# Optimization experiments

Measured on AMD Instinct MI355X. Metric: run time of the kernel, lower is better.

Reference implementation:

```python
import jax, jax.numpy as jnp
import numpy as np
from jax.scipy.special import logsumexp

B, T, D = 16, 512, 768
S, H, O = 4, 48, 48
EMISS_W = 0.5  # args.emiss_nn_weight


def setup_inputs() -> dict:
    key = jax.random.key(0)
    ks = jax.random.split(key, 6)
    emb = jax.random.normal(ks[0], (B, T, D), jnp.float32)
    # obs must be valid per-source distributions over n_obs (log is taken)
    obs = jax.nn.softmax(2.0 * jax.random.normal(ks[1], (B, T, S, O), jnp.float32), axis=-1)
    # default prior init: priors = 0.001, priors[0] = 1, param = log(priors)
    p = jnp.full((H,), 0.001, jnp.float32).at[0].set(1.0)
    state_priors = jnp.log(p)
    unnorm_trans = jax.random.normal(ks[2], (H, H), jnp.float32)
    unnorm_emiss = jnp.zeros((S, H, O), jnp.float32)
    # xavier_uniform with relu gain for the per-source emission Linears
    bound = np.sqrt(2.0) * np.sqrt(6.0 / (D + H * O))
    W_emiss = jax.random.uniform(ks[3], (S, H * O, D), jnp.float32, -bound, bound)
    b_emiss = jnp.zeros((S, H * O), jnp.float32)
    seq_lengths = jax.random.randint(ks[4], (B,), T // 2, T + 1).astype(jnp.int32)
    seq_lengths = seq_lengths.at[0].set(T)  # max length == T
    return dict(emb=emb, obs=obs, state_priors=state_priors, unnorm_trans=unnorm_trans,
                unnorm_emiss=unnorm_emiss, W_emiss=W_emiss, b_emiss=b_emiss,
                seq_lengths=seq_lengths)


def _lognorm(x):
    return x - logsumexp(x, axis=-1, keepdims=True)


def reference(emb, obs, state_priors, unnorm_trans, unnorm_emiss, W_emiss, b_emiss, seq_lengths):
    lp = jax.nn.log_softmax(state_priors)                 # [H]
    log_trans = jax.nn.log_softmax(unnorm_trans, axis=-1)  # [H,H] (constant over b,t)
    emiss = jax.nn.softmax(unnorm_emiss, axis=-1)          # [S,H,O]

    # neural emissions: per-source Linear(d_emb -> H*O), softmax over O
    logits = jnp.einsum('btd,sod->btso', emb, W_emiss) + b_emiss  # [B,T,S,H*O]
    nn_emiss = jax.nn.softmax(logits.reshape(B, T, S, H, O), axis=-1)
    # (nn_trans is computed by NeuralModule in the original but discarded)

    log_emiss = jnp.log((1.0 - EMISS_W) * emiss[None, None] + EMISS_W * nn_emiss)  # [B,T,S,H,O]
    # log_matmul over obs axis, then sum over sources -> [B,T,H]
    lep = logsumexp(log_emiss + jnp.log(obs)[:, :, :, None, :], axis=-1).sum(axis=2)

    # forward recursion (normalized each step)
    a0 = _lognorm(lp + lep[:, 0])                          # [B,H]

    def fstep(a_prev, lep_t):
        a = _lognorm(lep_t + logsumexp(a_prev[:, :, None] + log_trans[None], axis=1))
        return a, a

    _, alphas = jax.lax.scan(fstep, a0, jnp.swapaxes(lep[:, 1:], 0, 1))
    log_alpha = jnp.concatenate([a0[:, None], jnp.swapaxes(alphas, 0, 1)], axis=1)  # [B,T,H]

    # backward recursion: beta[t] = logsumexp_j(trans[i,j] + lep[t,j] + beta[t+1,j])
    bT = jnp.zeros((B, H), lep.dtype)

    def bstep(b_next, lep_t):
        b = logsumexp(log_trans[None] + (lep_t + b_next)[:, None, :], axis=2)
        return b, b

    _, betas = jax.lax.scan(bstep, bT, jnp.swapaxes(lep[:, :T - 1], 0, 1), reverse=True)
    log_beta = jnp.concatenate([jnp.swapaxes(betas, 0, 1), bT[:, None]], axis=1)  # [B,T,H]
    # per-example roll by (length - T) along time, as in the original
    log_beta = jax.vmap(lambda b, s: jnp.roll(b, s, axis=0))(log_beta, seq_lengths - T)

    log_gamma = _lognorm(log_alpha + log_beta)             # [B,T,H]

    # xi_t = trans + alpha[t-1] (outer-sum) (lep[t] + beta[t]),  t = 1..T-1
    xi = (log_trans[None, None]
          + log_alpha[:, :-1, :, None]
          + (lep[:, 1:] + log_beta[:, 1:])[:, :, None, :])  # [B,T-1,H,H]
    xi = xi - logsumexp(xi, axis=(-2, -1), keepdims=True)

    log_prior = jnp.mean(jnp.sum(jnp.exp(log_gamma[:, 0]) * lp, axis=-1))

    tran_terms = jnp.sum(jnp.exp(xi) * log_trans[None, None], axis=(-2, -1))  # [B,T-1]
    mask_tr = (jnp.arange(T - 1)[None] < (seq_lengths - 1)[:, None]).astype(lep.dtype)
    log_tran = jnp.mean(jnp.sum(tran_terms * mask_tr, axis=1))

    emis_terms = jnp.sum(jnp.exp(log_gamma) * lep, axis=-1)  # [B,T]
    mask_em = (jnp.arange(T)[None] < seq_lengths[:, None]).astype(lep.dtype)
    log_emis = jnp.mean(jnp.sum(emis_terms * mask_em, axis=1))

    return log_prior + log_tran + log_emis
```

## Files before the change

kernel.cpp:

```cpp
#include <hip/hip_runtime.h>
#include <math.h>

namespace {

constexpr int Bn = 16, Tn = 512, Dn = 768, Sn = 4, Hn = 48, On = 48;
constexpr int Mn = Bn * Tn;
constexpr int Gn = Sn * Hn;
constexpr int Nn = Gn * On;
constexpr float EMISS_W = 0.5f;

constexpr size_t OFF_LP   = 0;
constexpr size_t OFF_LT   = 64;
constexpr size_t OFF_PT   = OFF_LT + Hn*Hn;
constexpr size_t OFF_EM   = OFF_PT + Hn*Hn;
constexpr size_t OFF_LEPP = OFF_EM + (size_t)Sn*Hn*On;
constexpr size_t OFF_LEP  = OFF_LEPP + (size_t)Mn*Gn;
constexpr size_t OFF_LA   = OFF_LEP + (size_t)Mn*Hn;
constexpr size_t OFF_LB   = OFF_LA + (size_t)Mn*Hn;
constexpr size_t OFF_RED  = OFF_LB + (size_t)Mn*Hn;
constexpr size_t FLOATS_END = OFF_RED + (size_t)Mn;

typedef __attribute__((ext_vector_type(8))) short short8;
typedef __attribute__((ext_vector_type(4))) float f32x4;

__device__ inline float waveSum(float v){
#pragma unroll
  for (int o = 32; o; o >>= 1) v += __shfl_xor(v, o);
  return v;
}

__device__ inline unsigned short f2bf(float f){
  unsigned int u = __float_as_uint(f);
  u += 0x7FFFu + ((u >> 16) & 1u);
  return (unsigned short)(u >> 16);
}

__device__ inline void gload_lds16(const void* g, void* l){
  __builtin_amdgcn_global_load_lds(
      (const __attribute__((address_space(1))) void*)g,
      (__attribute__((address_space(3))) void*)l, 16, 0, 0);
}

__global__ void conv_kernel(const float* __restrict__ srcA, unsigned short* __restrict__ dstA,
                            int n4a,
                            const float* __restrict__ srcB, unsigned short* __restrict__ dstB,
                            int n4b){
  int i = blockIdx.x * blockDim.x + threadIdx.x;
  const float* s; unsigned short* d; int k;
  if (i < n4a){ s = srcA; d = dstA; k = i; }
  else { k = i - n4a; if (k >= n4b) return; s = srcB; d = dstB; }
  float4 v = ((const float4*)s)[k];
  ushort4 r;
  r.x = f2bf(v.x); r.y = f2bf(v.y); r.z = f2bf(v.z); r.w = f2bf(v.w);
  ((ushort4*)d)[k] = r;
}

__global__ void prep_kernel(const float* __restrict__ sp, const float* __restrict__ ut,
                            const float* __restrict__ ue, float* __restrict__ ws){
  int tid = threadIdx.x;
  float m = -INFINITY;
  for (int h = 0; h < Hn; ++h) m = fmaxf(m, sp[h]);
  float s = 0.f;
  for (int h = 0; h < Hn; ++h) s += __expf(sp[h] - m);
  float lse = m + __logf(s);
  if (tid < Hn) ws[OFF_LP + tid] = sp[tid] - lse;
  if (tid < Hn){
    const float* row = ut + tid * Hn;
    float mm = -INFINITY;
    for (int j = 0; j < Hn; ++j) mm = fmaxf(mm, row[j]);
    float ss = 0.f;
    for (int j = 0; j < Hn; ++j) ss += __expf(row[j] - mm);
    float l = mm + __logf(ss);
    for (int j = 0; j < Hn; ++j){
      float v = row[j] - l;
      ws[OFF_LT + tid*Hn + j] = v;
      ws[OFF_PT + tid*Hn + j] = __expf(v);
    }
  }
  for (int r = tid; r < Sn*Hn; r += blockDim.x){
    const float* row = ue + (size_t)r * On;
    float mm = -INFINITY;
    for (int o = 0; o < On; ++o) mm = fmaxf(mm, row[o]);
    float ss = 0.f;
    for (int o = 0; o < On; ++o) ss += __expf(row[o] - mm);
    float inv = 1.f/ss;
    for (int o = 0; o < On; ++o) ws[OFF_EM + (size_t)r*On + o] = __expf(row[o]-mm)*inv;
  }
}

constexpr int MT = 128, NT2 = 96, KT = 64;

__global__ __launch_bounds__(256) void gemm_lep_kernel(
    const unsigned short* __restrict__ embB, const unsigned short* __restrict__ WB,
    const float* __restrict__ bm, const float* __restrict__ obs,
    float* __restrict__ ws){
  __shared__ __align__(16) char smem[128*97*4];
  __shared__ float bias_s[96], em_s[96];
  const int tid = threadIdx.x, lane = tid & 63, w = tid >> 6;
  const int m0 = blockIdx.x * MT;
  const int N0 = blockIdx.y * NT2;
  if (tid < 96){
    bias_s[tid] = bm[N0 + tid];
    em_s[tid]   = ws[OFF_EM + N0 + tid];
  }
  const int wm = w & 1, wn = w >> 1;
  const int lm = lane & 15, q = lane >> 4;
  const int key = lm & 7;
  const int srow = lane >> 3, spc = lane & 7;

  f32x4 acc[4][3];
#pragma unroll
  for (int i=0;i<4;++i)
#pragma unroll
    for (int j=0;j<3;++j) acc[i][j] = (f32x4){0.f,0.f,0.f,0.f};

  for (int kc = 0; kc < Dn; kc += KT){
    __syncthreads();
#pragma unroll
    for (int i=0;i<4;++i){
      int idx = w*4 + i;
      int row = idx*8 + srow;
      int lc  = spc ^ (row & 7);
      gload_lds16(embB + (size_t)(m0+row)*Dn + kc + lc*8, smem + idx*1024);
    }
#pragma unroll
    for (int i=0;i<3;++i){
      int idx = w*3 + i;
      int row = idx*8 + srow;
      int lc  = spc ^ (row & 7);
      gload_lds16(WB + (size_t)(N0+row)*Dn + kc + lc*8, smem + 16384 + idx*1024);
    }
    __syncthreads();
#pragma unroll
    for (int s = 0; s < 2; ++s){
      short8 af[4], bf[3];
#pragma unroll
      for (int i=0;i<4;++i){
        int row = wm*64 + i*16 + lm;
        af[i] = *(const short8*)(smem + row*128 + (((s*4+q) ^ key) * 16));
      }
#pragma unroll
      for (int j=0;j<3;++j){
        int row = wn*48 + j*16 + lm;
        bf[j] = *(const short8*)(smem + 16384 + row*128 + (((s*4+q) ^ key) * 16));
      }
#pragma unroll
      for (int i=0;i<4;++i)
#pragma unroll
        for (int j=0;j<3;++j)
          acc[i][j] = __builtin_amdgcn_mfma_f32_16x16x32_bf16(af[i], bf[j], acc[i][j], 0, 0, 0);
    }
  }
  __syncthreads();
  float* C = (float*)smem;
#pragma unroll
  for (int i=0;i<4;++i)
#pragma unroll
    for (int j=0;j<3;++j)
#pragma unroll
      for (int r=0;r<4;++r){
        int mrow = wm*64 + i*16 + q*4 + r;
        int ncol = wn*48 + j*16 + lm;
        C[mrow*97 + ncol] = acc[i][j][r];
      }
  __syncthreads();
  {
    const int row = tid >> 1, half = tid & 1;
    const int m = m0 + row;
    const int g = N0/48 + half;
    const int s2 = g / Hn;
    const float* crow = C + row*97 + half*48;
    const float* ob   = obs + ((size_t)m*Sn + s2)*On;
    const float* bi   = bias_s + half*48;
    const float* em   = em_s + half*48;
    float Z=0.f, pd=0.f, eo=0.f;
#pragma unroll
    for (int o=0;o<On;++o){
      float e = __expf(crow[o] + bi[o]);
      float obv = ob[o];
      Z += e;
      pd = fmaf(e, obv, pd);
      eo = fmaf(em[o], obv, eo);
    }
    float val = __logf((1.f-EMISS_W)*eo + EMISS_W*(pd/Z));
    ws[OFF_LEPP + (size_t)m*Gn + g] = val;
  }
}

__global__ void lep_reduce_kernel(float* __restrict__ ws){
  int x = blockIdx.x * blockDim.x + threadIdx.x;
  if (x < Mn*Hn){
    int m = x / Hn, h = x - m*Hn;
    const size_t base = OFF_LEPP + (size_t)m*Gn + h;
    ws[OFF_LEP + x] = ws[base] + ws[base + Hn] + ws[base + 2*Hn] + ws[base + 3*Hn];
  }
}

constexpr int FBW = 40;
constexpr int FBL = 32;

__global__ __launch_bounds__(64) void fb_kernel(float* __restrict__ ws){
  __shared__ __align__(16) float ldsE[72*48];
  __shared__ __align__(16) float ring[2][64];
  const int lane = threadIdx.x;
  const int c    = blockIdx.x;
  const int b    = blockIdx.y;
  const bool fwd = blockIdx.z == 0;
  const bool act = lane < Hn;
  const int t0 = c*FBL, te = t0 + FBL - 1;

  float pt[Hn];
#pragma unroll
  for (int i = 0; i < Hn; ++i)
    pt[i] = act ? (fwd ? ws[OFF_PT + i*Hn + lane] : ws[OFF_PT + lane*Hn + i]) : 0.f;

  int row_lo, nrows, sA, sZ;
  bool exact;
  if (fwd){
    sA = t0 - FBW;
    exact = (sA < 1);
    row_lo = exact ? 0 : sA;
    if (exact) sA = 1;
    sZ = te;
    nrows = te - row_lo + 1;
  } else {
    int th = te + 1 + FBW;
    exact = (th > 510);
    sA = exact ? 510 : th - 1;
    sZ = t0;
    row_lo = t0;
    nrows = sA - t0 + 1;
  }

  {
    const float4* src = (const float4*)(ws + OFF_LEP + ((size_t)b*Tn + row_lo)*Hn);
    int n4 = nrows * (Hn/4);
    for (int i = lane; i < n4; i += 64){
      float4 v = src[i];
      float4 e;
      e.x = __expf(v.x); e.y = __expf(v.y); e.z = __expf(v.z); e.w = __expf(v.w);
      ((float4*)ldsE)[i] = e;
    }
  }
  __syncthreads();

  if (fwd){
    const size_t laF = OFF_LA + (size_t)b * Tn * Hn;
    float v;
    if (exact){
      v = act ? __expf(ws[OFF_LP + lane]) * ldsE[lane] : 0.f;
      if (c == 0 && act) ws[laF + lane] = v;
    } else {
      v = act ? 1.f : 0.f;
    }
    if (act) ring[0][lane] = v;
    __syncthreads();
    int cur = 0;
    for (int t = sA; t <= sZ; ++t){
      float S = waveSum(v);
      const float* rp = ring[cur];
      float s0=0.f,s1=0.f,s2=0.f,s3=0.f;
#pragma unroll
      for (int i = 0; i < Hn; i += 4){
        float4 a = *(const float4*)(rp + i);
        s0 = fmaf(a.x, pt[i+0], s0); s1 = fmaf(a.y, pt[i+1], s1);
        s2 = fmaf(a.z, pt[i+2], s2); s3 = fmaf(a.w, pt[i+3], s3);
      }
      float sd = (s0+s1)+(s2+s3);
      float e = act ? ldsE[(t - row_lo)*Hn + lane] : 0.f;
      float vn = act ? e * sd * (1.f/S) : 0.f;
      cur ^= 1;
      if (act) ring[cur][lane] = vn;
      __syncthreads();
      if (act && t >= t0) ws[laF + (size_t)t*Hn + lane] = vn;
      v = vn;
    }
  } else {
    const size_t lbF = OFF_LB + (size_t)b * Tn * Hn;
    float v = act ? 1.f : 0.f;
    if (exact && c == (Tn/FBL - 1) && act) ws[lbF + (size_t)(Tn-1)*Hn + lane] = 1.f;
    int cur = 0;
    for (int t = sA; t >= sZ; --t){
      float e = act ? ldsE[(t - row_lo)*Hn + lane] : 0.f;
      float wv = e * v;
      if (act) ring[cur][lane] = wv;
      float S = waveSum(wv);
      __syncthreads();
      const float* rp = ring[cur];
      float s0=0.f,s1=0.f,s2=0.f,s3=0.f;
#pragma unroll
      for (int j = 0; j < Hn; j += 4){
        float4 a = *(const float4*)(rp + j);
        s0 = fmaf(a.x, pt[j+0], s0); s1 = fmaf(a.y, pt[j+1], s1);
        s2 = fmaf(a.z, pt[j+2], s2); s3 = fmaf(a.w, pt[j+3], s3);
      }
      float vn = act ? ((s0+s1)+(s2+s3)) * (1.f/S) : 0.f;
      cur ^= 1;
      if (act && t <= te) ws[lbF + (size_t)t*Hn + lane] = vn;
      v = vn;
    }
  }
}

__global__ __launch_bounds__(256) void gamma_xi_kernel(
    const float* __restrict__ ws_c, float* __restrict__ ws,
    const int* __restrict__ seq_len){
  __shared__ float y_s[Hn], lap_s[Hn];
  __shared__ float red[8];
  const int tid = threadIdx.x;
  const int bid = blockIdx.x;
  const int b = bid >> 9, t = bid & (Tn-1);
  const int len = seq_len[b];
  int tb = t + (Tn - len); if (tb >= Tn) tb -= Tn;
  const size_t bt = (size_t)b*Tn + t;
  if (tid < Hn){
    float lb  = ws_c[OFF_LB + ((size_t)b*Tn + tb)*Hn + tid];
    float lep = ws_c[OFF_LEP + bt*Hn + tid];
    y_s[tid] = __expf(lep) * lb;
    if (t >= 1) lap_s[tid] = ws_c[OFF_LA + (bt-1)*Hn + tid];
  }
  float emis_term = 0.f, prior_term = 0.f;
  if (tid < 64){
    int h = (tid < Hn) ? tid : 0;
    float la  = ws_c[OFF_LA + bt*Hn + h];
    float lb  = ws_c[OFF_LB + ((size_t)b*Tn + tb)*Hn + h];
    float lep = ws_c[OFF_LEP + bt*Hn + h];
    float lp  = ws_c[OFF_LP + h];
    float wgt = (tid < Hn) ? la*lb : 0.f;
    float Z = waveSum(wgt);
    float inv = 1.f / Z;
    emis_term  = waveSum(wgt * lep) * inv;
    prior_term = waveSum(wgt * lp) * inv;
  }
  __syncthreads();
  float tran_term = 0.f;
  if (t >= 1){
    float se = 0.f, st = 0.f;
#pragma unroll
    for (int k=0;k<9;++k){
      int e = tid + k*256;
      int i = e / Hn, j = e - i*Hn;
      float e2 = ws_c[OFF_PT + e] * lap_s[i] * y_s[j];
      se += e2;
      st = fmaf(e2, ws_c[OFF_LT + e], st);
    }
    se = waveSum(se);
    st = waveSum(st);
    const int wid = tid >> 6;
    if ((tid & 63) == 0){ red[wid] = se; red[4+wid] = st; }
    __syncthreads();
    if (tid == 0){
      float SE = red[0]+red[1]+red[2]+red[3];
      float ST = red[4]+red[5]+red[6]+red[7];
      tran_term = ST / SE;
    }
  }
  if (tid == 0){
    float tot = 0.f;
    if (t < len)            tot += emis_term;
    if (t == 0)             tot += prior_term;
    if (t >= 1 && t < len)  tot += tran_term;
    ws[OFF_RED + bid] = tot;
  }
}

__global__ __launch_bounds__(256) void sum_kernel(const float* __restrict__ ws,
                                                  float* __restrict__ out){
  __shared__ float red[4];
  const int tid = threadIdx.x;
  float s = 0.f;
  for (int i = tid; i < Mn; i += 256) s += ws[OFF_RED + i];
  s = waveSum(s);
  if ((tid & 63) == 0) red[tid >> 6] = s;
  __syncthreads();
  if (tid == 0) out[0] = (red[0]+red[1]+red[2]+red[3]) * (1.f / Bn);
}

}

extern "C" void kernel_launch(void* const* d_in, const int* in_sizes, int n_in,
                              void* d_out, int out_size, void* d_ws, size_t ws_size,
                              hipStream_t stream){
  const float* emb = (const float*)d_in[0];
  const float* obs = (const float*)d_in[1];
  const float* sp  = (const float*)d_in[2];
  const float* ut  = (const float*)d_in[3];
  const float* ue  = (const float*)d_in[4];
  const float* Wm  = (const float*)d_in[5];
  const float* bm  = (const float*)d_in[6];
  const int*   sl  = (const int*)d_in[7];
  float* ws  = (float*)d_ws;
  float* out = (float*)d_out;
  (void)in_sizes; (void)n_in; (void)ws_size; (void)out_size;

  unsigned short* embB = (unsigned short*)(ws + FLOATS_END);
  unsigned short* WB   = embB + (size_t)Mn * Dn;

  const int n4a = Mn*Dn/4, n4b = Nn*Dn/4;
  conv_kernel<<<(n4a + n4b + 255)/256, 256, 0, stream>>>(emb, embB, n4a, Wm, WB, n4b);
  prep_kernel<<<1, 256, 0, stream>>>(sp, ut, ue, ws);
  gemm_lep_kernel<<<dim3(Mn/MT, Nn/NT2), 256, 0, stream>>>(embB, WB, bm, obs, ws);
  lep_reduce_kernel<<<(Mn*Hn + 255)/256, 256, 0, stream>>>(ws);
  fb_kernel<<<dim3(Tn/FBL, Bn, 2), 64, 0, stream>>>(ws);
  gamma_xi_kernel<<<Bn*Tn, 256, 0, stream>>>(ws, ws, sl);
  sum_kernel<<<1, 256, 0, stream>>>(ws, out);
}
```

Baseline: 322.0 us.

## Widen GEMM N-tile to 192 with two-pass epilogue; shrink forward-backward chunks

The emission GEMM tile grows from 128x96 to 128x192, so each A tile loaded from embeddings is reused across twice as many output columns and the grid halves along N. The epilogue now stages the two 96-column halves through shared memory in two passes so the existing LDS buffer still fits, which adds barriers and doubles accumulator registers. The windowed forward-backward kernel also uses shorter chunks (16) and warmup windows (24), giving more blocks and less redundant recurrence per block, but truncating the approximate warmup window, which may affect accuracy.

```diff
diff --git a/kernel.cpp b/kernel.cpp
--- a/kernel.cpp
+++ b/kernel.cpp
@@ -88,18 +88,18 @@
   }
 }
 
-constexpr int MT = 128, NT2 = 96, KT = 64;
+constexpr int MT = 128, NTB = 192, KT = 64;
 
 __global__ __launch_bounds__(256) void gemm_lep_kernel(
     const unsigned short* __restrict__ embB, const unsigned short* __restrict__ WB,
     const float* __restrict__ bm, const float* __restrict__ obs,
     float* __restrict__ ws){
   __shared__ __align__(16) char smem[128*97*4];
-  __shared__ float bias_s[96], em_s[96];
+  __shared__ float bias_s[NTB], em_s[NTB];
   const int tid = threadIdx.x, lane = tid & 63, w = tid >> 6;
   const int m0 = blockIdx.x * MT;
-  const int N0 = blockIdx.y * NT2;
-  if (tid < 96){
+  const int N0 = blockIdx.y * NTB;
+  if (tid < NTB){
     bias_s[tid] = bm[N0 + tid];
     em_s[tid]   = ws[OFF_EM + N0 + tid];
   }
@@ -108,11 +108,11 @@
   const int key = lm & 7;
   const int srow = lane >> 3, spc = lane & 7;
 
-  f32x4 acc[4][3];
+  f32x4 acc[4][6];
 #pragma unroll
   for (int i=0;i<4;++i)
 #pragma unroll
-    for (int j=0;j<3;++j) acc[i][j] = (f32x4){0.f,0.f,0.f,0.f};
+    for (int j=0;j<6;++j) acc[i][j] = (f32x4){0.f,0.f,0.f,0.f};
 
   for (int kc = 0; kc < Dn; kc += KT){
     __syncthreads();
@@ -124,8 +124,8 @@
       gload_lds16(embB + (size_t)(m0+row)*Dn + kc + lc*8, smem + idx*1024);
     }
 #pragma unroll
-    for (int i=0;i<3;++i){
-      int idx = w*3 + i;
+    for (int i=0;i<6;++i){
+      int idx = w*6 + i;
       int row = idx*8 + srow;
       int lc  = spc ^ (row & 7);
       gload_lds16(WB + (size_t)(N0+row)*Dn + kc + lc*8, smem + 16384 + idx*1024);
@@ -133,57 +133,63 @@
     __syncthreads();
 #pragma unroll
     for (int s = 0; s < 2; ++s){
-      short8 af[4], bf[3];
+      short8 af[4], bf[6];
 #pragma unroll
       for (int i=0;i<4;++i){
         int row = wm*64 + i*16 + lm;
         af[i] = *(const short8*)(smem + row*128 + (((s*4+q) ^ key) * 16));
       }
 #pragma unroll
-      for (int j=0;j<3;++j){
-        int row = wn*48 + j*16 + lm;
+      for (int j=0;j<6;++j){
+        int row = wn*96 + j*16 + lm;
         bf[j] = *(const short8*)(smem + 16384 + row*128 + (((s*4+q) ^ key) * 16));
       }
 #pragma unroll
       for (int i=0;i<4;++i)
 #pragma unroll
-        for (int j=0;j<3;++j)
+        for (int j=0;j<6;++j)
           acc[i][j] = __builtin_amdgcn_mfma_f32_16x16x32_bf16(af[i], bf[j], acc[i][j], 0, 0, 0);
     }
   }
   __syncthreads();
   float* C = (float*)smem;
 #pragma unroll
-  for (int i=0;i<4;++i)
-#pragma unroll
-    for (int j=0;j<3;++j)
-#pragma unroll
-      for (int r=0;r<4;++r){
-        int mrow = wm*64 + i*16 + q*4 + r;
-        int ncol = wn*48 + j*16 + lm;
-        C[mrow*97 + ncol] = acc[i][j][r];
+  for (int p = 0; p < 2; ++p){
+    if (wn == p){
+#pragma unroll
+      for (int i=0;i<4;++i)
+#pragma unroll
+        for (int j=0;j<6;++j)
+#pragma unroll
+          for (int r=0;r<4;++r){
+            int mrow = wm*64 + i*16 + q*4 + r;
+            int ncol = j*16 + lm;
+            C[mrow*97 + ncol] = acc[i][j][r];
+          }
+    }
+    __syncthreads();
+    {
+      const int row = tid >> 1, half = tid & 1;
+      const int m = m0 + row;
+      const int g = N0/48 + p*2 + half;
+      const int s2 = g / Hn;
+      const float* crow = C + row*97 + half*48;
+      const float* ob   = obs + ((size_t)m*Sn + s2)*On;
+      const float* bi   = bias_s + p*96 + half*48;
+      const float* em   = em_s + p*96 + half*48;
+      float Z=0.f, pd=0.f, eo=0.f;
+#pragma unroll
+      for (int o=0;o<On;++o){
+        float e = __expf(crow[o] + bi[o]);
+        float obv = ob[o];
+        Z += e;
+        pd = fmaf(e, obv, pd);
+        eo = fmaf(em[o], obv, eo);
       }
-  __syncthreads();
-  {
-    const int row = tid >> 1, half = tid & 1;
-    const int m = m0 + row;
-    const int g = N0/48 + half;
-    const int s2 = g / Hn;
-    const float* crow = C + row*97 + half*48;
-    const float* ob   = obs + ((size_t)m*Sn + s2)*On;
-    const float* bi   = bias_s + half*48;
-    const float* em   = em_s + half*48;
-    float Z=0.f, pd=0.f, eo=0.f;
-#pragma unroll
-    for (int o=0;o<On;++o){
-      float e = __expf(crow[o] + bi[o]);
-      float obv = ob[o];
-      Z += e;
-      pd = fmaf(e, obv, pd);
-      eo = fmaf(em[o], obv, eo);
-    }
-    float val = __logf((1.f-EMISS_W)*eo + EMISS_W*(pd/Z));
-    ws[OFF_LEPP + (size_t)m*Gn + g] = val;
+      float val = __logf((1.f-EMISS_W)*eo + EMISS_W*(pd/Z));
+      ws[OFF_LEPP + (size_t)m*Gn + g] = val;
+    }
+    __syncthreads();
   }
 }
 
@@ -196,11 +202,11 @@
   }
 }
 
-constexpr int FBW = 40;
-constexpr int FBL = 32;
+constexpr int FBW = 24;
+constexpr int FBL = 16;
 
 __global__ __launch_bounds__(64) void fb_kernel(float* __restrict__ ws){
-  __shared__ __align__(16) float ldsE[72*48];
+  __shared__ __align__(16) float ldsE[(FBW+FBL)*48];
   __shared__ __align__(16) float ring[2][64];
   const int lane = threadIdx.x;
   const int c    = blockIdx.x;
@@ -225,8 +231,8 @@
     nrows = te - row_lo + 1;
   } else {
     int th = te + 1 + FBW;
-    exact = (th > 510);
-    sA = exact ? 510 : th - 1;
+    exact = (th > Tn - 2);
+    sA = exact ? Tn - 2 : th - 1;
     sZ = t0;
     row_lo = t0;
     nrows = sA - t0 + 1;
@@ -399,7 +405,7 @@
   const int n4a = Mn*Dn/4, n4b = Nn*Dn/4;
   conv_kernel<<<(n4a + n4b + 255)/256, 256, 0, stream>>>(emb, embB, n4a, Wm, WB, n4b);
   prep_kernel<<<1, 256, 0, stream>>>(sp, ut, ue, ws);
-  gemm_lep_kernel<<<dim3(Mn/MT, Nn/NT2), 256, 0, stream>>>(embB, WB, bm, obs, ws);
+  gemm_lep_kernel<<<dim3(Mn/MT, Nn/NTB), 256, 0, stream>>>(embB, WB, bm, obs, ws);
   lep_reduce_kernel<<<(Mn*Hn + 255)/256, 256, 0, stream>>>(ws);
   fb_kernel<<<dim3(Tn/FBL, Bn, 2), 64, 0, stream>>>(ws);
   gamma_xi_kernel<<<Bn*Tn, 256, 0, stream>>>(ws, ws, sl);
```

Measured after the change: 306.0 us. -5.0%, faster.
